# Kernel tuning notes

Measured on AMD Instinct MI355X. Metric: run time of the kernel, lower is better.

The kernel has to match this reference:

```python
import jax, jax.numpy as jnp
import numpy as np

B, T, D, H, R, K = 64, 2048, 256, 256, 64, 8
NUM_LEVELS = 5  # height of the 8-ary tree over 2048 nodes (levels 0..4)


def _gru(x, h, w_ih, w_hh, b_ih, b_hh):
    # torch.nn.GRUCell math
    gi = x @ w_ih.T + b_ih          # [N, 3H]
    gh = h @ w_hh.T + b_hh          # [N, 3H]
    i_r, i_z, i_n = jnp.split(gi, 3, axis=-1)
    h_r, h_z, h_n = jnp.split(gh, 3, axis=-1)
    r = jax.nn.sigmoid(i_r + h_r)
    z = jax.nn.sigmoid(i_z + h_z)
    n = jnp.tanh(i_n + r * h_n)
    return (1.0 - z) * n + z * h


def setup_inputs() -> dict:
    key = jax.random.key(0)
    ks = jax.random.split(key, 11)
    s = 1.0 / np.sqrt(H)
    embs = jax.random.normal(ks[0], (B, T, D), jnp.float32)
    rel_emb = (jax.random.normal(ks[1], (R, D), jnp.float32) * s).at[0].set(0.0)  # padding_idx=0
    node_w_ih = jax.random.uniform(ks[2], (3 * H, D), jnp.float32, -s, s)
    node_w_hh = jax.random.uniform(ks[3], (3 * H, H), jnp.float32, -s, s)
    node_b_ih = jax.random.uniform(ks[4], (3 * H,), jnp.float32, -s, s)
    node_b_hh = jax.random.uniform(ks[5], (3 * H,), jnp.float32, -s, s)
    rel_w_ih = jax.random.uniform(ks[6], (3 * H, D), jnp.float32, -s, s)
    rel_w_hh = jax.random.uniform(ks[7], (3 * H, H), jnp.float32, -s, s)
    rel_b_ih = jax.random.uniform(ks[8], (3 * H,), jnp.float32, -s, s)
    rel_b_hh = jax.random.uniform(ks[9], (3 * H,), jnp.float32, -s, s)
    # Deterministic 8-ary tree per batch element: node t>=1 has parent (t-1)//K, root has -1.
    par = np.full(T, -1, np.int64)
    par[1:] = (np.arange(1, T) - 1) // K
    level = np.zeros(T, np.int64)  # topological level = 1 + max level of children (leaves = 0)
    for t in range(T - 1, 0, -1):
        level[par[t]] = max(level[par[t]], level[t] + 1)
    parents = jnp.tile(jnp.asarray(par, jnp.int32)[None, :], (B, 1))
    levels = jnp.tile(jnp.asarray(level, jnp.int32)[None, :], (B, 1))
    rels = jax.random.randint(ks[10], (B, T), 1, R, jnp.int32)
    return dict(embs=embs, rel_emb=rel_emb,
                node_w_ih=node_w_ih, node_w_hh=node_w_hh, node_b_ih=node_b_ih, node_b_hh=node_b_hh,
                rel_w_ih=rel_w_ih, rel_w_hh=rel_w_hh, rel_b_ih=rel_b_ih, rel_b_hh=rel_b_hh,
                parents=parents, rels=rels, levels=levels)


def reference(embs, rel_emb, node_w_ih, node_w_hh, node_b_ih, node_b_hh,
              rel_w_ih, rel_w_hh, rel_b_ih, rel_b_hh, parents, rels, levels):
    b, t, d = embs.shape
    n = b * t
    x = embs.reshape(n, d)                       # node input features
    par = parents.reshape(n).astype(jnp.int32)
    lev = levels.reshape(n, 1)
    # one (potential) edge per node: child -> parent; roots (par == -1) scatter to dummy bin n
    batch_off = (jnp.arange(n, dtype=jnp.int32) // t) * t
    dst = jnp.where(par >= 0, batch_off + par, n)
    rel_x = rel_emb[rels.reshape(n)]             # edge feature = rel embedding of child's relation

    h = jnp.zeros((n, H), embs.dtype)
    # per-level topological propagation (DGL prop_nodes): leaves first, root last
    for L in range(NUM_LEVELS):
        msg = _gru(rel_x, h, rel_w_ih, rel_w_hh, rel_b_ih, rel_b_hh)   # message along each edge
        red = jax.ops.segment_sum(msg, dst, num_segments=n + 1)[:n]    # mailbox sum at parents
        h_new = _gru(x, red, node_w_ih, node_w_hh, node_b_ih, node_b_hh)
        h = jnp.where(lev == L, h_new, h)        # only nodes at this topological level update
    return h.reshape(b, t, H)
```

## Files before the change

### kernel.cpp

```cpp
#include <hip/hip_runtime.h>
#include <hip/hip_bf16.h>
#include <cstdint>
#include <cstddef>

#define B_ 64
#define T_ 2048

typedef unsigned short ushort_t;
typedef __attribute__((ext_vector_type(8))) short bf16x8;
typedef __attribute__((ext_vector_type(4))) float f32x4;

__device__ __forceinline__ float sigmoidf_(float x){ return 1.f/(1.f+__expf(-x)); }
__device__ __forceinline__ float tanhf_(float x){
  x = fminf(fmaxf(x,-15.f),15.f);
  float e = __expf(2.f*x);
  return (e-1.f)/(e+1.f);
}

__device__ __forceinline__ unsigned f2b_pair(float lo, float hi){
  unsigned a = __float_as_uint(lo), b = __float_as_uint(hi);
  a += 0x7FFFu + ((a>>16)&1u);
  b += 0x7FFFu + ((b>>16)&1u);
  return (a>>16) | (b & 0xFFFF0000u);
}
__device__ __forceinline__ uint4 pack8(float4 x, float4 y){
  uint4 v;
  v.x = f2b_pair(x.x, x.y);
  v.y = f2b_pair(x.z, x.w);
  v.z = f2b_pair(y.x, y.y);
  v.w = f2b_pair(y.z, y.w);
  return v;
}

__global__ __launch_bounds__(256)
void table_kernel(const float* __restrict__ rel_emb, const float* __restrict__ w_ih,
                  const float* __restrict__ b_ih, float* __restrict__ table)
{
  int idx = blockIdx.x*256 + threadIdx.x;
  int r = idx/768, j = idx - r*768;
  const float* e = rel_emb + (size_t)r*256;
  const float* w = w_ih   + (size_t)j*256;
  float acc = 0.f;
  for(int k=0;k<256;k+=4){
    float4 ev = *(const float4*)(e+k);
    float4 wv = *(const float4*)(w+k);
    acc = fmaf(ev.x,wv.x,acc); acc = fmaf(ev.y,wv.y,acc);
    acc = fmaf(ev.z,wv.z,acc); acc = fmaf(ev.w,wv.w,acc);
  }
  table[idx] = acc + b_ih[j];
}

__global__ __launch_bounds__(256)
void wcvt_kernel(const float* __restrict__ a, const float* __restrict__ b, const float* __restrict__ c,
                 ushort_t* __restrict__ oa, ushort_t* __restrict__ ob, ushort_t* __restrict__ oc)
{
  int i = blockIdx.x*256 + threadIdx.x;
  int seg = i / 24576;
  int off = (i - seg*24576) * 8;
  const float* s; ushort_t* d;
  if(seg==0){ s=a; d=oa; } else if(seg==1){ s=b; d=ob; } else { s=c; d=oc; }
  float4 x = *(const float4*)(s+off), y = *(const float4*)(s+off+4);
  *(uint4*)(d+off) = pack8(x,y);
}


template<bool LEAF>
__global__ __launch_bounds__(256)
void node_mfma(const float* __restrict__ embs, const float* __restrict__ red,
               const ushort_t* __restrict__ wih, const ushort_t* __restrict__ whh,
               const float* __restrict__ b_ih, const float* __restrict__ b_hh,
               float* __restrict__ out, int t_lo, unsigned cnt, unsigned Mtot)
{
  __shared__ ushort_t As[128][32];
  __shared__ ushort_t Bs[192][32];
  const int tid  = threadIdx.x;
  const unsigned Mbase = blockIdx.x*128u;
  const int nb   = blockIdx.y;
  const int lane = tid & 63, w = tid >> 6;
  const int quad = lane >> 4, cl = lane & 15;

  const int srow = tid >> 2;
  const int g8   = (tid & 3) * 8;
  unsigned r0 = Mbase + srow;      if(r0 > Mtot-1) r0 = Mtot-1;
  unsigned r1 = Mbase + srow + 64; if(r1 > Mtot-1) r1 = Mtot-1;
  unsigned b0v = r0 / cnt, t0v = (unsigned)t_lo + (r0 - b0v*cnt);
  unsigned b1v = r1 / cnt, t1v = (unsigned)t_lo + (r1 - b1v*cnt);
  const float* x0p = embs + ((size_t)b0v*T_ + t0v)*256 + g8;
  const float* x1p = embs + ((size_t)b1v*T_ + t1v)*256 + g8;
  const float* rd0p = red + ((size_t)b0v*256 + t0v)*256 + g8;
  const float* rd1p = red + ((size_t)b1v*256 + t1v)*256 + g8;
  const size_t woff0 = ((size_t)(0*256 + nb*64 + srow))*256 + g8;
  const size_t woff1 = ((size_t)(1*256 + nb*64 + srow))*256 + g8;
  const size_t woff2 = ((size_t)(2*256 + nb*64 + srow))*256 + g8;

  f32x4 acc[2][12];
  f32x4 accN2[2][4];
  const f32x4 zz = {0.f,0.f,0.f,0.f};
  #pragma unroll
  for(int i=0;i<2;i++){
    #pragma unroll
    for(int j=0;j<12;j++) acc[i][j] = zz;
    #pragma unroll
    for(int j=0;j<4;j++) accN2[i][j] = zz;
  }

  const int npass = LEAF ? 1 : 2;
  for(int pass=0; pass<npass; pass++){
    const float* a0 = pass ? rd0p : x0p;
    const float* a1 = pass ? rd1p : x1p;
    const ushort_t* W = pass ? whh : wih;
    #pragma unroll 1
    for(int kk=0; kk<256; kk+=32){
      float4 ax0 = *(const float4*)(a0 + kk);
      float4 ay0 = *(const float4*)(a0 + kk + 4);
      float4 ax1 = *(const float4*)(a1 + kk);
      float4 ay1 = *(const float4*)(a1 + kk + 4);
      uint4 w0 = *(const uint4*)(W + woff0 + kk);
      uint4 w1 = *(const uint4*)(W + woff1 + kk);
      uint4 w2 = *(const uint4*)(W + woff2 + kk);
      __syncthreads();
      *(uint4*)&As[srow     ][g8] = pack8(ax0, ay0);
      *(uint4*)&As[srow + 64][g8] = pack8(ax1, ay1);
      *(uint4*)&Bs[srow      ][g8] = w0;
      *(uint4*)&Bs[srow +  64][g8] = w1;
      *(uint4*)&Bs[srow + 128][g8] = w2;
      __syncthreads();
      bf16x8 af0 = *(const bf16x8*)&As[w*32      + cl][quad*8];
      bf16x8 af1 = *(const bf16x8*)&As[w*32 + 16 + cl][quad*8];
      #pragma unroll
      for(int j=0;j<12;j++){
        bf16x8 bfj = *(const bf16x8*)&Bs[j*16 + cl][quad*8];
        if(!LEAF && pass==1 && j>=8){
          accN2[0][j-8] = __builtin_amdgcn_mfma_f32_16x16x32_bf16(af0, bfj, accN2[0][j-8], 0,0,0);
          accN2[1][j-8] = __builtin_amdgcn_mfma_f32_16x16x32_bf16(af1, bfj, accN2[1][j-8], 0,0,0);
        } else {
          acc[0][j] = __builtin_amdgcn_mfma_f32_16x16x32_bf16(af0, bfj, acc[0][j], 0,0,0);
          acc[1][j] = __builtin_amdgcn_mfma_f32_16x16x32_bf16(af1, bfj, acc[1][j], 0,0,0);
        }
      }
    }
  }

  float bir[4],biz[4],bin[4],bhr[4],bhz[4],bhn[4];
  #pragma unroll
  for(int c=0;c<4;c++){
    int col = nb*64 + c*16 + cl;
    bir[c]=b_ih[col]; biz[c]=b_ih[256+col]; bin[c]=b_ih[512+col];
    bhr[c]=b_hh[col]; bhz[c]=b_hh[256+col]; bhn[c]=b_hh[512+col];
  }
  #pragma unroll
  for(int i=0;i<2;i++){
    #pragma unroll
    for(int r=0;r<4;r++){
      unsigned gm = Mbase + (unsigned)(w*32 + i*16 + quad*4 + r);
      if(gm > Mtot-1) gm = Mtot-1;
      unsigned b = gm / cnt, t = (unsigned)t_lo + (gm - b*cnt);
      float* orow = out + ((size_t)b*T_ + t)*256;
      const float* rr = red + ((size_t)b*256 + t)*256;
      #pragma unroll
      for(int c=0;c<4;c++){
        int col = nb*64 + c*16 + cl;
        float gr = acc[i][c][r]   + bir[c] + bhr[c];
        float gz = acc[i][4+c][r] + biz[c] + bhz[c];
        float gni = acc[i][8+c][r] + bin[c];
        float hn  = (LEAF ? 0.f : accN2[i][c][r]) + bhn[c];
        float rg = sigmoidf_(gr);
        float zg = sigmoidf_(gz);
        float ng = tanhf_(gni + rg*hn);
        float rv = LEAF ? 0.f : rr[col];
        orow[col] = (1.f-zg)*ng + zg*rv;
      }
    }
  }
}

__global__ __launch_bounds__(256)
void msg_mfma(const float* __restrict__ hbuf, const ushort_t* __restrict__ wbf,
              const float* __restrict__ b_hh, const float* __restrict__ table,
              const int* __restrict__ rels, float* __restrict__ red,
              int t_lo, unsigned cnt, unsigned Mtot)
{
  __shared__ ushort_t As[128][32];
  __shared__ ushort_t Bs[192][32];
  const int tid  = threadIdx.x;
  const unsigned Mbase = blockIdx.x*128u;
  const int nb   = blockIdx.y;
  const int lane = tid & 63, w = tid >> 6;
  const int quad = lane >> 4, cl = lane & 15;

  const int srow = tid >> 2;
  const int g8   = (tid & 3) * 8;
  unsigned r0 = Mbase + srow;      if(r0 > Mtot-1) r0 = Mtot-1;
  unsigned r1 = Mbase + srow + 64; if(r1 > Mtot-1) r1 = Mtot-1;
  unsigned b0v = r0 / cnt, t0v = (unsigned)t_lo + (r0 - b0v*cnt);
  unsigned b1v = r1 / cnt, t1v = (unsigned)t_lo + (r1 - b1v*cnt);
  const float* a0 = hbuf + ((size_t)b0v*T_ + t0v)*256 + g8;
  const float* a1 = hbuf + ((size_t)b1v*T_ + t1v)*256 + g8;
  const size_t woff0 = ((size_t)(0*256 + nb*64 + srow))*256 + g8;
  const size_t woff1 = ((size_t)(1*256 + nb*64 + srow))*256 + g8;
  const size_t woff2 = ((size_t)(2*256 + nb*64 + srow))*256 + g8;

  f32x4 acc[2][12];
  const f32x4 zz = {0.f,0.f,0.f,0.f};
  #pragma unroll
  for(int i=0;i<2;i++)
    #pragma unroll
    for(int j=0;j<12;j++) acc[i][j] = zz;

  #pragma unroll 1
  for(int kk=0; kk<256; kk+=32){
    float4 ax0 = *(const float4*)(a0 + kk);
    float4 ay0 = *(const float4*)(a0 + kk + 4);
    float4 ax1 = *(const float4*)(a1 + kk);
    float4 ay1 = *(const float4*)(a1 + kk + 4);
    uint4 w0 = *(const uint4*)(wbf + woff0 + kk);
    uint4 w1 = *(const uint4*)(wbf + woff1 + kk);
    uint4 w2 = *(const uint4*)(wbf + woff2 + kk);
    __syncthreads();
    *(uint4*)&As[srow     ][g8] = pack8(ax0, ay0);
    *(uint4*)&As[srow + 64][g8] = pack8(ax1, ay1);
    *(uint4*)&Bs[srow      ][g8] = w0;
    *(uint4*)&Bs[srow +  64][g8] = w1;
    *(uint4*)&Bs[srow + 128][g8] = w2;
    __syncthreads();
    bf16x8 af0 = *(const bf16x8*)&As[w*32      + cl][quad*8];
    bf16x8 af1 = *(const bf16x8*)&As[w*32 + 16 + cl][quad*8];
    #pragma unroll
    for(int j=0;j<12;j++){
      bf16x8 bfj = *(const bf16x8*)&Bs[j*16 + cl][quad*8];
      acc[0][j] = __builtin_amdgcn_mfma_f32_16x16x32_bf16(af0, bfj, acc[0][j], 0,0,0);
      acc[1][j] = __builtin_amdgcn_mfma_f32_16x16x32_bf16(af1, bfj, acc[1][j], 0,0,0);
    }
  }

  float bhr[4],bhz[4],bhn[4];
  #pragma unroll
  for(int c=0;c<4;c++){
    int col = nb*64 + c*16 + cl;
    bhr[c]=b_hh[col]; bhz[c]=b_hh[256+col]; bhn[c]=b_hh[512+col];
  }
  #pragma unroll
  for(int i=0;i<2;i++){
    #pragma unroll
    for(int r=0;r<4;r++){
      unsigned gm = Mbase + (unsigned)(w*32 + i*16 + quad*4 + r);
      bool ok = (gm < Mtot);
      if(gm > Mtot-1) gm = Mtot-1;
      unsigned b = gm / cnt, t = (unsigned)t_lo + (gm - b*cnt);
      int rel = rels[(size_t)b*T_ + t];
      const float* tb = table + (size_t)rel*768;
      const float* hr = hbuf + ((size_t)b*T_ + t)*256;
      float* rd = red + ((size_t)b*256 + ((t-1)>>3))*256;
      #pragma unroll
      for(int c=0;c<4;c++){
        int col = nb*64 + c*16 + cl;
        float gr  = tb[col]     + acc[i][c][r]   + bhr[c];
        float gz  = tb[256+col] + acc[i][4+c][r] + bhz[c];
        float gnh = acc[i][8+c][r] + bhn[c];
        float rg = sigmoidf_(gr);
        float zg = sigmoidf_(gz);
        float ng = tanhf_(tb[512+col] + rg*gnh);
        float msg = (1.f-zg)*ng + zg*hr[col];
        if(ok) atomicAdd(rd + col, msg);
      }
    }
  }
}

extern "C" void kernel_launch(void* const* d_in, const int* in_sizes, int n_in,
                              void* d_out, int out_size, void* d_ws, size_t ws_size,
                              hipStream_t stream)
{
  const float* embs    = (const float*)d_in[0];
  const float* rel_emb = (const float*)d_in[1];
  const float* nwih    = (const float*)d_in[2];
  const float* nwhh    = (const float*)d_in[3];
  const float* nbih    = (const float*)d_in[4];
  const float* nbhh    = (const float*)d_in[5];
  const float* rwih    = (const float*)d_in[6];
  const float* rwhh    = (const float*)d_in[7];
  const float* rbih    = (const float*)d_in[8];
  const float* rbhh    = (const float*)d_in[9];
  const int*   rels    = (const int*)d_in[11];
  float* out = (float*)d_out;

  float* red   = (float*)d_ws;
  float* table = red + (size_t)4194304;
  ushort_t* wih_bf  = (ushort_t*)(table + 49152);
  ushort_t* whh_bf  = wih_bf + 196608;
  ushort_t* rwhh_bf = whh_bf + 196608;

  hipMemsetAsync(red, 0, (size_t)4194304*4, stream);
  table_kernel<<<dim3(192), 256, 0, stream>>>(rel_emb, rwih, rbih, table);
  wcvt_kernel<<<dim3(288), 256, 0, stream>>>(nwih, nwhh, rwhh, wih_bf, whh_bf, rwhh_bf);

  const int      tlo[5] = {256, 32, 4, 1, 0};
  const unsigned cntv[5]= {1792, 224, 28, 3, 1};
  const unsigned Mv[5]  = {114688, 14336, 1792, 192, 64};

  for(int L=0; L<5; L++){
    dim3 g((Mv[L]+127)/128, 4);
    if(L==0)
      node_mfma<true ><<<g, 256, 0, stream>>>(embs, red, wih_bf, whh_bf, nbih, nbhh, out, tlo[L], cntv[L], Mv[L]);
    else
      node_mfma<false><<<g, 256, 0, stream>>>(embs, red, wih_bf, whh_bf, nbih, nbhh, out, tlo[L], cntv[L], Mv[L]);
    if(L < 4)
      msg_mfma<<<g, 256, 0, stream>>>(out, rwhh_bf, rbhh, table, rels, red, tlo[L], cntv[L], Mv[L]);
  }
}
```

Before: 884.6 us.

## Prefetch next K-tile into registers, pad LDS rows, pre-reduce atomics by parent

Both GEMM kernels now issue the global loads for the next 32-wide K slice right after the LDS barrier, so the memory latency overlaps the MFMA work on the current slice. In the node kernel the two-pass loop is flattened into one 512-step stream. LDS rows are padded from 32 to 40 elements to reduce bank conflicts on fragment reads. In the message kernel, rows that share a parent are summed in registers before a single atomicAdd, which cuts atomic traffic at the cost of more live registers.

```diff
diff --git a/kernel.cpp b/kernel.cpp
--- a/kernel.cpp
+++ b/kernel.cpp
@@ -5,6 +5,7 @@
 
 #define B_ 64
 #define T_ 2048
+#define LDP 40
 
 typedef unsigned short ushort_t;
 typedef __attribute__((ext_vector_type(8))) short bf16x8;
@@ -71,8 +72,8 @@
                const float* __restrict__ b_ih, const float* __restrict__ b_hh,
                float* __restrict__ out, int t_lo, unsigned cnt, unsigned Mtot)
 {
-  __shared__ ushort_t As[128][32];
-  __shared__ ushort_t Bs[192][32];
+  __shared__ ushort_t As[128][LDP];
+  __shared__ ushort_t Bs[192][LDP];
   const int tid  = threadIdx.x;
   const unsigned Mbase = blockIdx.x*128u;
   const int nb   = blockIdx.y;
@@ -104,42 +105,48 @@
     for(int j=0;j<4;j++) accN2[i][j] = zz;
   }
 
-  const int npass = LEAF ? 1 : 2;
-  for(int pass=0; pass<npass; pass++){
-    const float* a0 = pass ? rd0p : x0p;
-    const float* a1 = pass ? rd1p : x1p;
-    const ushort_t* W = pass ? whh : wih;
-    #pragma unroll 1
-    for(int kk=0; kk<256; kk+=32){
-      float4 ax0 = *(const float4*)(a0 + kk);
-      float4 ay0 = *(const float4*)(a0 + kk + 4);
-      float4 ax1 = *(const float4*)(a1 + kk);
-      float4 ay1 = *(const float4*)(a1 + kk + 4);
-      uint4 w0 = *(const uint4*)(W + woff0 + kk);
-      uint4 w1 = *(const uint4*)(W + woff1 + kk);
-      uint4 w2 = *(const uint4*)(W + woff2 + kk);
-      __syncthreads();
-      *(uint4*)&As[srow     ][g8] = pack8(ax0, ay0);
-      *(uint4*)&As[srow + 64][g8] = pack8(ax1, ay1);
-      *(uint4*)&Bs[srow      ][g8] = w0;
-      *(uint4*)&Bs[srow +  64][g8] = w1;
-      *(uint4*)&Bs[srow + 128][g8] = w2;
-      __syncthreads();
-      bf16x8 af0 = *(const bf16x8*)&As[w*32      + cl][quad*8];
-      bf16x8 af1 = *(const bf16x8*)&As[w*32 + 16 + cl][quad*8];
-      #pragma unroll
-      for(int j=0;j<12;j++){
-        bf16x8 bfj = *(const bf16x8*)&Bs[j*16 + cl][quad*8];
-        if(!LEAF && pass==1 && j>=8){
-          accN2[0][j-8] = __builtin_amdgcn_mfma_f32_16x16x32_bf16(af0, bfj, accN2[0][j-8], 0,0,0);
-          accN2[1][j-8] = __builtin_amdgcn_mfma_f32_16x16x32_bf16(af1, bfj, accN2[1][j-8], 0,0,0);
-        } else {
-          acc[0][j] = __builtin_amdgcn_mfma_f32_16x16x32_bf16(af0, bfj, acc[0][j], 0,0,0);
-          acc[1][j] = __builtin_amdgcn_mfma_f32_16x16x32_bf16(af1, bfj, acc[1][j], 0,0,0);
-        }
+  const int KSTOT = LEAF ? 256 : 512;
+  float4 ax0,ay0,ax1,ay1; uint4 w0,w1,w2;
+
+#define NLOAD(KS) do{ \
+    const int kk_ = (KS) & 255; \
+    const float* A0_ = (LEAF || (KS) < 256) ? x0p : rd0p; \
+    const float* A1_ = (LEAF || (KS) < 256) ? x1p : rd1p; \
+    const ushort_t* W_ = (LEAF || (KS) < 256) ? wih : whh; \
+    ax0 = *(const float4*)(A0_+kk_); ay0 = *(const float4*)(A0_+kk_+4); \
+    ax1 = *(const float4*)(A1_+kk_); ay1 = *(const float4*)(A1_+kk_+4); \
+    w0 = *(const uint4*)(W_+woff0+kk_); \
+    w1 = *(const uint4*)(W_+woff1+kk_); \
+    w2 = *(const uint4*)(W_+woff2+kk_); \
+  }while(0)
+
+  NLOAD(0);
+  #pragma unroll 1
+  for(int ks=0; ks<KSTOT; ks+=32){
+    __syncthreads();
+    *(uint4*)&As[srow     ][g8] = pack8(ax0, ay0);
+    *(uint4*)&As[srow + 64][g8] = pack8(ax1, ay1);
+    *(uint4*)&Bs[srow      ][g8] = w0;
+    *(uint4*)&Bs[srow +  64][g8] = w1;
+    *(uint4*)&Bs[srow + 128][g8] = w2;
+    __syncthreads();
+    if(ks + 32 < KSTOT) NLOAD(ks + 32);
+    const bool p1 = (!LEAF) && (ks >= 256);
+    bf16x8 af0 = *(const bf16x8*)&As[w*32      + cl][quad*8];
+    bf16x8 af1 = *(const bf16x8*)&As[w*32 + 16 + cl][quad*8];
+    #pragma unroll
+    for(int j=0;j<12;j++){
+      bf16x8 bfj = *(const bf16x8*)&Bs[j*16 + cl][quad*8];
+      if(j>=8 && p1){
+        accN2[0][j-8] = __builtin_amdgcn_mfma_f32_16x16x32_bf16(af0, bfj, accN2[0][j-8], 0,0,0);
+        accN2[1][j-8] = __builtin_amdgcn_mfma_f32_16x16x32_bf16(af1, bfj, accN2[1][j-8], 0,0,0);
+      } else {
+        acc[0][j] = __builtin_amdgcn_mfma_f32_16x16x32_bf16(af0, bfj, acc[0][j], 0,0,0);
+        acc[1][j] = __builtin_amdgcn_mfma_f32_16x16x32_bf16(af1, bfj, acc[1][j], 0,0,0);
       }
     }
   }
+#undef NLOAD
 
   float bir[4],biz[4],bin[4],bhr[4],bhz[4],bhn[4];
   #pragma unroll
@@ -180,8 +187,8 @@
               const int* __restrict__ rels, float* __restrict__ red,
               int t_lo, unsigned cnt, unsigned Mtot)
 {
-  __shared__ ushort_t As[128][32];
-  __shared__ ushort_t Bs[192][32];
+  __shared__ ushort_t As[128][LDP];
+  __shared__ ushort_t Bs[192][LDP];
   const int tid  = threadIdx.x;
   const unsigned Mbase = blockIdx.x*128u;
   const int nb   = blockIdx.y;
@@ -207,15 +214,19 @@
     #pragma unroll
     for(int j=0;j<12;j++) acc[i][j] = zz;
 
+  float4 ax0,ay0,ax1,ay1; uint4 w0,w1,w2;
+
+#define MLOAD(KK) do{ \
+    ax0 = *(const float4*)(a0+(KK)); ay0 = *(const float4*)(a0+(KK)+4); \
+    ax1 = *(const float4*)(a1+(KK)); ay1 = *(const float4*)(a1+(KK)+4); \
+    w0 = *(const uint4*)(wbf+woff0+(KK)); \
+    w1 = *(const uint4*)(wbf+woff1+(KK)); \
+    w2 = *(const uint4*)(wbf+woff2+(KK)); \
+  }while(0)
+
+  MLOAD(0);
   #pragma unroll 1
   for(int kk=0; kk<256; kk+=32){
-    float4 ax0 = *(const float4*)(a0 + kk);
-    float4 ay0 = *(const float4*)(a0 + kk + 4);
-    float4 ax1 = *(const float4*)(a1 + kk);
-    float4 ay1 = *(const float4*)(a1 + kk + 4);
-    uint4 w0 = *(const uint4*)(wbf + woff0 + kk);
-    uint4 w1 = *(const uint4*)(wbf + woff1 + kk);
-    uint4 w2 = *(const uint4*)(wbf + woff2 + kk);
     __syncthreads();
     *(uint4*)&As[srow     ][g8] = pack8(ax0, ay0);
     *(uint4*)&As[srow + 64][g8] = pack8(ax1, ay1);
@@ -223,6 +234,7 @@
     *(uint4*)&Bs[srow +  64][g8] = w1;
     *(uint4*)&Bs[srow + 128][g8] = w2;
     __syncthreads();
+    if(kk + 32 < 256) MLOAD(kk + 32);
     bf16x8 af0 = *(const bf16x8*)&As[w*32      + cl][quad*8];
     bf16x8 af1 = *(const bf16x8*)&As[w*32 + 16 + cl][quad*8];
     #pragma unroll
@@ -232,6 +244,7 @@
       acc[1][j] = __builtin_amdgcn_mfma_f32_16x16x32_bf16(af1, bfj, acc[1][j], 0,0,0);
     }
   }
+#undef MLOAD
 
   float bhr[4],bhz[4],bhn[4];
   #pragma unroll
@@ -241,27 +254,46 @@
   }
   #pragma unroll
   for(int i=0;i<2;i++){
+    float* rp[4]; bool okr[4]; const float* tb[4]; const float* hrp[4];
     #pragma unroll
     for(int r=0;r<4;r++){
       unsigned gm = Mbase + (unsigned)(w*32 + i*16 + quad*4 + r);
-      bool ok = (gm < Mtot);
+      okr[r] = (gm < Mtot);
       if(gm > Mtot-1) gm = Mtot-1;
       unsigned b = gm / cnt, t = (unsigned)t_lo + (gm - b*cnt);
       int rel = rels[(size_t)b*T_ + t];
-      const float* tb = table + (size_t)rel*768;
-      const float* hr = hbuf + ((size_t)b*T_ + t)*256;
-      float* rd = red + ((size_t)b*256 + ((t-1)>>3))*256;
+      tb[r]  = table + (size_t)rel*768;
+      hrp[r] = hbuf + ((size_t)b*T_ + t)*256;
+      rp[r]  = red + ((size_t)b*256 + ((t-1)>>3))*256;
+    }
+    float mv[4][4];
+    #pragma unroll
+    for(int r=0;r<4;r++){
       #pragma unroll
       for(int c=0;c<4;c++){
         int col = nb*64 + c*16 + cl;
-        float gr  = tb[col]     + acc[i][c][r]   + bhr[c];
-        float gz  = tb[256+col] + acc[i][4+c][r] + bhz[c];
+        float gr  = tb[r][col]     + acc[i][c][r]   + bhr[c];
+        float gz  = tb[r][256+col] + acc[i][4+c][r] + bhz[c];
         float gnh = acc[i][8+c][r] + bhn[c];
         float rg = sigmoidf_(gr);
         float zg = sigmoidf_(gz);
-        float ng = tanhf_(tb[512+col] + rg*gnh);
-        float msg = (1.f-zg)*ng + zg*hr[col];
-        if(ok) atomicAdd(rd + col, msg);
+        float ng = tanhf_(tb[r][512+col] + rg*gnh);
+        mv[r][c] = (1.f-zg)*ng + zg*hrp[r][col];
+      }
+    }
+    #pragma unroll
+    for(int c=0;c<4;c++){
+      int col = nb*64 + c*16 + cl;
+      float a = 0.f; bool any = false;
+      #pragma unroll
+      for(int r=0;r<4;r++){
+        if(okr[r]){ a += mv[r][c]; any = true; }
+        bool flush;
+        if(r==3) flush = true; else flush = (rp[r+1] != rp[r]);
+        if(flush){
+          if(any) atomicAdd(rp[r] + col, a);
+          a = 0.f; any = false;
+        }
       }
     }
   }
```

Result: faster. 717.4 us (-18.9%).
